# Optimization experiments

Hardware: AMD Instinct MI355X
Metric: run time of the kernel (lower is better)

## Reference

```python
import jax, jax.numpy as jnp
import numpy as np

# dims: T tokens, H hidden, E experts, I expert intermediate, K top-k
T, H, E, I, K = 2048, 1024, 64, 768, 8


def setup_inputs() -> dict:
    key = jax.random.key(0)
    k0, k1, k2, k3, k4 = jax.random.split(key, 5)
    s = 0.02  # init scale
    return {
        "hidden_states": jax.random.normal(k0, (T, H), jnp.float32),
        "w_router": jax.random.normal(k1, (E, H), jnp.float32) * s,   # gate (router) Linear, no bias
        "w_gate": jax.random.normal(k2, (E, I, H), jnp.float32) * s,  # per-expert gate_proj (out,in)
        "w_up": jax.random.normal(k3, (E, I, H), jnp.float32) * s,    # per-expert up_proj
        "w_down": jax.random.normal(k4, (E, H, I), jnp.float32) * s,  # per-expert down_proj
    }


def reference(hidden_states, w_router, w_gate, w_up, w_down):
    x = hidden_states  # (T, H)
    # --- router: softmax scores, top-k selection, renormalize (select_experts, softmax scoring) ---
    router_logits = jnp.einsum("th,eh->te", x, w_router)          # (T, E)
    probs = jax.nn.softmax(router_logits, axis=-1)
    topk_w, topk_ids = jax.lax.top_k(probs, K)                     # (T, K)
    topk_w = topk_w / jnp.sum(topk_w, axis=-1, keepdims=True)      # renormalize=True
    # scatter per-slot weights into a (T, E) combine matrix (zero for unselected experts)
    route = jnp.zeros((x.shape[0], E), x.dtype)
    route = route.at[jnp.arange(x.shape[0])[:, None], topk_ids].add(topk_w)
    # --- experts: SwiGLU MLP per expert, weighted combine (FusedMoE dispatch/combine) ---
    g = jnp.einsum("th,eih->tei", x, w_gate)                       # (T, E, I)
    u = jnp.einsum("th,eih->tei", x, w_up)
    h = jax.nn.silu(g) * u
    y = jnp.einsum("tei,ehi,te->th", h, w_down, route)             # weighted scatter-combine
    return y
```

## Files before the change

### kernel.cpp

```cpp
#include <hip/hip_runtime.h>
#include <hip/hip_bf16.h>
#include <cstdint>
#include <cstddef>

#define T_TOK 2048
#define H_DIM 1024
#define E_NUM 64
#define I_DIM 768
#define K_TOP 8

typedef __attribute__((ext_vector_type(8))) __bf16 bf16x8;
typedef __attribute__((ext_vector_type(8))) unsigned short u16x8;
typedef __attribute__((ext_vector_type(4))) float f32x4;
typedef unsigned short ushort_t;

__device__ __forceinline__ unsigned short f2bf(float f) {
  uint32_t u = __builtin_bit_cast(uint32_t, f);
  u += 0x7fffu + ((u >> 16) & 1u);
  return (unsigned short)(u >> 16);
}

__device__ __forceinline__ u16x8 cvt8b(f32x4 a, f32x4 b) {
  bf16x8 r;
  r[0] = (__bf16)a[0]; r[1] = (__bf16)a[1]; r[2] = (__bf16)a[2]; r[3] = (__bf16)a[3];
  r[4] = (__bf16)b[0]; r[5] = (__bf16)b[1]; r[6] = (__bf16)b[2]; r[7] = (__bf16)b[3];
  return __builtin_bit_cast(u16x8, r);
}

__device__ __forceinline__ void async16(const void* l, const void* g) {
  __builtin_amdgcn_global_load_lds(
      (const __attribute__((address_space(1))) unsigned int*)g,
      (__attribute__((address_space(3))) unsigned int*)l, 16, 0, 0);
}

__device__ __forceinline__ int xcd_decode(int wg0, int n_act) {
  int q = n_act >> 3, r = n_act & 7;
  int xcd = wg0 & 7, rank = wg0 >> 3;
  int cnt = q + (xcd < r ? 1 : 0);
  if (rank >= cnt) return -1;
  return (xcd < r ? xcd * (q + 1) : r * (q + 1) + (xcd - r) * q) + rank;
}

__global__ __launch_bounds__(256) void xcast_kernel(const float* __restrict__ x,
                                                    ushort_t* __restrict__ xb) {
  int i = blockIdx.x * 256 + threadIdx.x;
  const f32x4* s = (const f32x4*)(x + (size_t)i * 8);
  *(u16x8*)(xb + (size_t)i * 8) = cvt8b(s[0], s[1]);
}

__global__ __launch_bounds__(64) void router_kernel(
    const float* __restrict__ x, const float* __restrict__ wr,
    int* __restrict__ topk_id, float* __restrict__ topk_w,
    int* __restrict__ counts) {
  const int t0 = blockIdx.x * 4;
  const int e = threadIdx.x;
  const float4* wv = (const float4*)(wr + (size_t)e * H_DIM);
  const float4* xv0 = (const float4*)(x + (size_t)t0 * H_DIM);
  const float4* xv1 = (const float4*)(x + (size_t)(t0 + 1) * H_DIM);
  const float4* xv2 = (const float4*)(x + (size_t)(t0 + 2) * H_DIM);
  const float4* xv3 = (const float4*)(x + (size_t)(t0 + 3) * H_DIM);
  float acc0 = 0.f, acc1 = 0.f, acc2 = 0.f, acc3 = 0.f;
#pragma unroll 4
  for (int i = 0; i < H_DIM / 4; ++i) {
    float4 b = wv[i];
    float4 a0 = xv0[i], a1 = xv1[i], a2 = xv2[i], a3 = xv3[i];
    acc0 = fmaf(a0.x, b.x, fmaf(a0.y, b.y, fmaf(a0.z, b.z, fmaf(a0.w, b.w, acc0))));
    acc1 = fmaf(a1.x, b.x, fmaf(a1.y, b.y, fmaf(a1.z, b.z, fmaf(a1.w, b.w, acc1))));
    acc2 = fmaf(a2.x, b.x, fmaf(a2.y, b.y, fmaf(a2.z, b.z, fmaf(a2.w, b.w, acc2))));
    acc3 = fmaf(a3.x, b.x, fmaf(a3.y, b.y, fmaf(a3.z, b.z, fmaf(a3.w, b.w, acc3))));
  }
  float accs[4] = {acc0, acc1, acc2, acc3};
#pragma unroll 1
  for (int tt = 0; tt < 4; ++tt) {
    int t = t0 + tt;
    float acc = accs[tt];
    float m = acc;
    for (int o = 32; o; o >>= 1) m = fmaxf(m, __shfl_xor(m, o));
    float p = __expf(acc - m);
    float s = p;
    for (int o = 32; o; o >>= 1) s += __shfl_xor(s, o);
    p /= s;
    float v = p;
    int sid = 0;
    float sw = 0.f;
    for (int k = 0; k < K_TOP; ++k) {
      float bv = v;
      int bi = e;
      for (int o = 32; o; o >>= 1) {
        float ov = __shfl_xor(bv, o);
        int oi = __shfl_xor(bi, o);
        if (ov > bv || (ov == bv && oi < bi)) { bv = ov; bi = oi; }
      }
      if (e == k) { sid = bi; sw = bv; }
      if (e == bi) v = -1.f;
    }
    float ssum = (e < K_TOP) ? sw : 0.f;
    for (int o = 32; o; o >>= 1) ssum += __shfl_xor(ssum, o);
    if (e < K_TOP) {
      topk_id[t * K_TOP + e] = sid;
      topk_w[t * K_TOP + e] = sw / ssum;
      atomicAdd(&counts[sid], 1);
    }
  }
}

__global__ __launch_bounds__(64) void scan_kernel(
    const int* __restrict__ counts, int* __restrict__ offsets,
    int* __restrict__ cursor, int* __restrict__ tile_list,
    int* __restrict__ n_tiles) {
  int e = threadIdx.x;
  int ne = counts[e];
  int x = ne;
  for (int o = 1; o < 64; o <<= 1) {
    int v = __shfl_up(x, o);
    if (e >= o) x += v;
  }
  int excl = x - ne;
  offsets[e] = excl;
  cursor[e] = excl;
  int ntl = (ne + 127) >> 7;
  if (ntl > 3) ntl = 3;
  int y2 = ntl;
  for (int o = 1; o < 64; o <<= 1) {
    int v = __shfl_up(y2, o);
    if (e >= o) y2 += v;
  }
  int texcl = y2 - ntl;
  for (int m = 0; m < ntl; ++m) tile_list[texcl + m] = (e << 2) | m;
  if (e == 63) *n_tiles = texcl + ntl;
}

__global__ __launch_bounds__(256) void build_kernel(
    const int* __restrict__ topk_id, const float* __restrict__ topk_w,
    int* __restrict__ cursor, int* __restrict__ pair_token, float* __restrict__ pair_w) {
  int i = blockIdx.x * 256 + threadIdx.x;
  int t = i >> 3;
  int e = topk_id[i];
  int pos = atomicAdd(&cursor[e], 1);
  pair_token[pos] = t;
  pair_w[pos] = topk_w[i];
}


#define GU_NIT 32

__global__ __launch_bounds__(256, 3) void gemm_gu_kernel(
    const ushort_t* __restrict__ xb, const float* __restrict__ wg,
    const float* __restrict__ wu, const int* __restrict__ offsets,
    const int* __restrict__ counts, const int* __restrict__ pair_token,
    const int* __restrict__ tile_list, const int* __restrict__ n_tiles,
    ushort_t* __restrict__ h_buf) {
  int idx = xcd_decode(blockIdx.x, (*n_tiles) * 12);
  if (idx < 0) return;
  int tl = idx / 12, nt = idx - tl * 12;
  int ent = tile_list[tl];
  int e = ent >> 2, mt = ent & 3;
  int ne = counts[e], off = offsets[e];
  int ib = nt * 64;
  int vr = ne - mt * 128;
  if (vr <= 0) return;
  if (vr > 128) vr = 128;

  __shared__ __align__(16) ushort_t Xs[128 * 32];
  __shared__ __align__(16) ushort_t Gs[64 * 32];
  __shared__ __align__(16) ushort_t Us[64 * 32];
  __shared__ int sTok[128];

  const int tid = threadIdx.x;
  const int lane = tid & 63;
  const int wid = tid >> 6;
  if (tid < 128) {
    int p = mt * 128 + tid;
    sTok[tid] = pair_token[off + (p < ne ? p : ne - 1)];
  }
  __syncthreads();

  const ushort_t* xsrc[2];
  int xdst[2];
#pragma unroll
  for (int j = 0; j < 2; ++j) {
    int p = j * 256 + tid;
    int row = p >> 2, c = p & 3;
    xsrc[j] = xb + (size_t)sTok[row] * H_DIM + ((c ^ ((row >> 1) & 3)) << 3);
    xdst[j] = (j * 256 + wid * 64) * 8;
  }
  const int wrow = tid >> 2, wc = tid & 3;
  const float* gsrc = wg + ((size_t)e * I_DIM + ib + wrow) * H_DIM + wc * 8;
  const float* usrc = wu + ((size_t)e * I_DIM + ib + wrow) * H_DIM + wc * 8;
  const int wdst = (wrow * 4 + (wc ^ ((wrow >> 1) & 3))) * 8;

  const int wrM = wid >> 1, wrN = wid & 1;
  const int lrow = lane & 15, lk = lane >> 4;
  const bool wact = (wrM * 64) < vr;

  f32x4 accG[4][2], accU[4][2];
#pragma unroll
  for (int mi = 0; mi < 4; ++mi)
#pragma unroll
    for (int ni = 0; ni < 2; ++ni) {
      accG[mi][ni] = f32x4{0.f, 0.f, 0.f, 0.f};
      accU[mi][ni] = f32x4{0.f, 0.f, 0.f, 0.f};
    }

#pragma unroll 1
  for (int k = 0; k < GU_NIT; ++k) {
    const int k0 = k * 32;
    async16(&Xs[xdst[0]], xsrc[0] + k0);
    async16(&Xs[xdst[1]], xsrc[1] + k0);
    {
      f32x4 g0 = *(const f32x4*)(gsrc + k0);
      f32x4 g1 = *(const f32x4*)(gsrc + k0 + 4);
      f32x4 u0 = *(const f32x4*)(usrc + k0);
      f32x4 u1 = *(const f32x4*)(usrc + k0 + 4);
      *(u16x8*)&Gs[wdst] = cvt8b(g0, g1);
      *(u16x8*)&Us[wdst] = cvt8b(u0, u1);
    }
    __syncthreads();
    if (wact) {
      bf16x8 af[4];
#pragma unroll
      for (int mi = 0; mi < 4; ++mi) {
        int r = wrM * 64 + mi * 16 + lrow;
        af[mi] = __builtin_bit_cast(
            bf16x8, *(const u16x8*)&Xs[r * 32 + ((lk ^ ((r >> 1) & 3)) << 3)]);
      }
#pragma unroll
      for (int ni = 0; ni < 2; ++ni) {
        int br = wrN * 32 + ni * 16 + lrow;
        int ci = br * 32 + ((lk ^ ((br >> 1) & 3)) << 3);
        bf16x8 bg = __builtin_bit_cast(bf16x8, *(const u16x8*)&Gs[ci]);
        bf16x8 bu = __builtin_bit_cast(bf16x8, *(const u16x8*)&Us[ci]);
#pragma unroll
        for (int mi = 0; mi < 4; ++mi) {
          accG[mi][ni] = __builtin_amdgcn_mfma_f32_16x16x32_bf16(af[mi], bg, accG[mi][ni], 0, 0, 0);
          accU[mi][ni] = __builtin_amdgcn_mfma_f32_16x16x32_bf16(af[mi], bu, accU[mi][ni], 0, 0, 0);
        }
      }
    }
    __syncthreads();
  }

#pragma unroll
  for (int mi = 0; mi < 4; ++mi)
#pragma unroll
    for (int ni = 0; ni < 2; ++ni)
#pragma unroll
      for (int r = 0; r < 4; ++r) {
        int grow = wrM * 64 + mi * 16 + lk * 4 + r;
        if (grow < vr) {
          int col = ib + wrN * 32 + ni * 16 + lrow;
          float g = accG[mi][ni][r], u = accU[mi][ni][r];
          float hv = g / (1.f + __expf(-g)) * u;
          h_buf[(size_t)(off + mt * 128 + grow) * I_DIM + col] = f2bf(hv);
        }
      }
}

#define DN_NIT 24

__global__ __launch_bounds__(256, 3) void gemm_down_kernel(
    const ushort_t* __restrict__ h_buf, const float* __restrict__ wd,
    const int* __restrict__ offsets, const int* __restrict__ counts,
    const int* __restrict__ pair_token, const float* __restrict__ pair_w,
    const int* __restrict__ tile_list, const int* __restrict__ n_tiles,
    float* __restrict__ y) {
  int idx = xcd_decode(blockIdx.x, (*n_tiles) * 8);
  if (idx < 0) return;
  int tl = idx >> 3, nt = idx & 7;
  int ent = tile_list[tl];
  int e = ent >> 2, mt = ent & 3;
  int ne = counts[e], off = offsets[e];
  int hb = nt * 128;
  int vr = ne - mt * 128;
  if (vr <= 0) return;
  if (vr > 128) vr = 128;

  __shared__ __align__(16) ushort_t Ah[128 * 32];
  __shared__ __align__(16) ushort_t Bs[128 * 32];
  __shared__ int sTok[128];
  __shared__ float sPw[128];

  const int tid = threadIdx.x;
  const int lane = tid & 63;
  const int wid = tid >> 6;
  if (tid < 128) {
    int p = mt * 128 + tid;
    int ix = off + (p < ne ? p : ne - 1);
    sTok[tid] = pair_token[ix];
    sPw[tid] = pair_w[ix];
  }
  __syncthreads();

  const ushort_t* asrc[2];
  int adst[2];
#pragma unroll
  for (int j = 0; j < 2; ++j) {
    int p = j * 256 + tid;
    int row = p >> 2, c = p & 3;
    int pr = mt * 128 + row;
    int hr = off + (pr < ne ? pr : ne - 1);
    asrc[j] = h_buf + (size_t)hr * I_DIM + ((c ^ ((row >> 1) & 3)) << 3);
    adst[j] = (j * 256 + wid * 64) * 8;
  }
  const int brow = tid >> 1, bc0 = (tid & 1) * 2, bc1 = bc0 + 1;
  const float* bsrc = wd + ((size_t)e * H_DIM + hb + brow) * I_DIM + bc0 * 8;
  const int bdst0 = (brow * 4 + (bc0 ^ ((brow >> 1) & 3))) * 8;
  const int bdst1 = (brow * 4 + (bc1 ^ ((brow >> 1) & 3))) * 8;

  const int wrM = wid >> 1, wrN = wid & 1;
  const int lrow = lane & 15, lk = lane >> 4;
  const bool wact = (wrM * 64) < vr;

  f32x4 acc[4][4];
#pragma unroll
  for (int mi = 0; mi < 4; ++mi)
#pragma unroll
    for (int ni = 0; ni < 4; ++ni) acc[mi][ni] = f32x4{0.f, 0.f, 0.f, 0.f};

#pragma unroll 1
  for (int k = 0; k < DN_NIT; ++k) {
    const int k0 = k * 32;
    async16(&Ah[adst[0]], asrc[0] + k0);
    async16(&Ah[adst[1]], asrc[1] + k0);
    {
      f32x4 b0 = *(const f32x4*)(bsrc + k0);
      f32x4 b1 = *(const f32x4*)(bsrc + k0 + 4);
      f32x4 b2 = *(const f32x4*)(bsrc + k0 + 8);
      f32x4 b3 = *(const f32x4*)(bsrc + k0 + 12);
      *(u16x8*)&Bs[bdst0] = cvt8b(b0, b1);
      *(u16x8*)&Bs[bdst1] = cvt8b(b2, b3);
    }
    __syncthreads();
    if (wact) {
      bf16x8 af[4];
#pragma unroll
      for (int mi = 0; mi < 4; ++mi) {
        int r = wrM * 64 + mi * 16 + lrow;
        af[mi] = __builtin_bit_cast(
            bf16x8, *(const u16x8*)&Ah[r * 32 + ((lk ^ ((r >> 1) & 3)) << 3)]);
      }
#pragma unroll
      for (int ni = 0; ni < 4; ++ni) {
        int br = wrN * 64 + ni * 16 + lrow;
        bf16x8 bb = __builtin_bit_cast(
            bf16x8, *(const u16x8*)&Bs[br * 32 + ((lk ^ ((br >> 1) & 3)) << 3)]);
#pragma unroll
        for (int mi = 0; mi < 4; ++mi)
          acc[mi][ni] = __builtin_amdgcn_mfma_f32_16x16x32_bf16(af[mi], bb, acc[mi][ni], 0, 0, 0);
      }
    }
    __syncthreads();
  }

#pragma unroll
  for (int mi = 0; mi < 4; ++mi)
#pragma unroll
    for (int ni = 0; ni < 4; ++ni)
#pragma unroll
      for (int r = 0; r < 4; ++r) {
        int grow = wrM * 64 + mi * 16 + lk * 4 + r;
        if (grow < vr) {
          int col = hb + wrN * 64 + ni * 16 + lrow;
          float val = acc[mi][ni][r] * sPw[grow];
          unsafeAtomicAdd(&y[(size_t)sTok[grow] * H_DIM + col], val);
        }
      }
}

extern "C" void kernel_launch(void* const* d_in, const int* in_sizes, int n_in,
                              void* d_out, int out_size, void* d_ws, size_t ws_size,
                              hipStream_t stream) {
  const float* x  = (const float*)d_in[0];
  const float* wr = (const float*)d_in[1];
  const float* wg = (const float*)d_in[2];
  const float* wu = (const float*)d_in[3];
  const float* wd = (const float*)d_in[4];
  float* y = (float*)d_out;

  char* ws = (char*)d_ws;
  int* counts    = (int*)(ws + 0);
  int* offsets   = (int*)(ws + 256);
  int* cursor    = (int*)(ws + 512);
  int* n_tiles   = (int*)(ws + 768);
  int* tile_list = (int*)(ws + 1024);
  int*   topk_id    = (int*)(ws + 2048);
  float* topk_w     = (float*)(ws + 2048 + 1 * 65536);
  int*   pair_token = (int*)(ws + 2048 + 2 * 65536);
  float* pair_w     = (float*)(ws + 2048 + 3 * 65536);
  ushort_t* h_buf = (ushort_t*)(ws + 2048 + 4 * 65536);
  ushort_t* xb = (ushort_t*)(ws + 2048 + 4 * 65536 + (size_t)T_TOK * I_DIM * K_TOP * 2);

  hipMemsetAsync(counts, 0, 256, stream);
  hipMemsetAsync(y, 0, (size_t)T_TOK * H_DIM * sizeof(float), stream);

  xcast_kernel<<<(T_TOK * H_DIM / 8) / 256, 256, 0, stream>>>(x, xb);
  router_kernel<<<T_TOK / 4, 64, 0, stream>>>(x, wr, topk_id, topk_w, counts);
  scan_kernel<<<1, 64, 0, stream>>>(counts, offsets, cursor, tile_list, n_tiles);
  build_kernel<<<(T_TOK * K_TOP) / 256, 256, 0, stream>>>(topk_id, topk_w, cursor, pair_token, pair_w);
  gemm_gu_kernel<<<E_NUM * 3 * 12, 256, 0, stream>>>(
      xb, wg, wu, offsets, counts, pair_token, tile_list, n_tiles, h_buf);
  gemm_down_kernel<<<E_NUM * 3 * 8, 256, 0, stream>>>(
      h_buf, wd, offsets, counts, pair_token, pair_w, tile_list, n_tiles, y);
}
```

Before: 412.7 us.

## Enlarge MoE GEMM tiles to 256 rows with 512-thread blocks and double-buffered LDS

Both expert GEMM kernels now use 512-thread blocks covering 256 routed rows. Gate-up tiles are 128 intermediate columns (gate and up stacked into one B tile, combined through LDS in the epilogue), and down tiles are 256 hidden columns. The K loop is double-buffered: the next X/H async copy and the fp32 weight loads are issued before the MFMAs on the current buffer, leaving one barrier per iteration. The aim is fewer fp32 weight re-reads per expert, since fewer M-tiles cover each expert, plus overlap of loads with compute. In exchange, LDS use rises to about 66 KB and register pressure grows, which lowers occupancy, and tiles are more padded when experts have few tokens.

```diff
diff --git a/kernel.cpp b/kernel.cpp
--- a/kernel.cpp
+++ b/kernel.cpp
@@ -118,8 +118,8 @@
   int excl = x - ne;
   offsets[e] = excl;
   cursor[e] = excl;
-  int ntl = (ne + 127) >> 7;
-  if (ntl > 3) ntl = 3;
+  int ntl = (ne + 255) >> 8;
+  if (ntl > 2) ntl = 2;
   int y2 = ntl;
   for (int o = 1; o < 64; o <<= 1) {
     int v = __shfl_up(y2, o);
@@ -144,33 +144,36 @@
 
 #define GU_NIT 32
 
-__global__ __launch_bounds__(256, 3) void gemm_gu_kernel(
+__global__ __launch_bounds__(512) void gemm_gu_kernel(
     const ushort_t* __restrict__ xb, const float* __restrict__ wg,
     const float* __restrict__ wu, const int* __restrict__ offsets,
     const int* __restrict__ counts, const int* __restrict__ pair_token,
     const int* __restrict__ tile_list, const int* __restrict__ n_tiles,
     ushort_t* __restrict__ h_buf) {
-  int idx = xcd_decode(blockIdx.x, (*n_tiles) * 12);
+  int idx = xcd_decode(blockIdx.x, (*n_tiles) * 6);
   if (idx < 0) return;
-  int tl = idx / 12, nt = idx - tl * 12;
+  int tl = idx / 6, nt = idx - tl * 6;
   int ent = tile_list[tl];
   int e = ent >> 2, mt = ent & 3;
   int ne = counts[e], off = offsets[e];
-  int ib = nt * 64;
-  int vr = ne - mt * 128;
+  int ib = nt * 128;
+  int vr = ne - mt * 256;
   if (vr <= 0) return;
-  if (vr > 128) vr = 128;
-
-  __shared__ __align__(16) ushort_t Xs[128 * 32];
-  __shared__ __align__(16) ushort_t Gs[64 * 32];
-  __shared__ __align__(16) ushort_t Us[64 * 32];
-  __shared__ int sTok[128];
+  if (vr > 256) vr = 256;
+
+  __shared__ __align__(16) char L[66560];
+  ushort_t* Xs = (ushort_t*)L;
+  ushort_t* Bl = (ushort_t*)(L + 32768);
+  int* sTok = (int*)(L + 65536);
 
   const int tid = threadIdx.x;
   const int lane = tid & 63;
   const int wid = tid >> 6;
-  if (tid < 128) {
-    int p = mt * 128 + tid;
+  const int wrM = wid >> 2, wrN = wid & 3;
+  const int lrow = lane & 15, lk = lane >> 4;
+
+  if (tid < 256) {
+    int p = mt * 256 + tid;
     sTok[tid] = pair_token[off + (p < ne ? p : ne - 1)];
   }
   __syncthreads();
@@ -179,112 +182,152 @@
   int xdst[2];
 #pragma unroll
   for (int j = 0; j < 2; ++j) {
-    int p = j * 256 + tid;
+    int p = j * 512 + tid;
     int row = p >> 2, c = p & 3;
     xsrc[j] = xb + (size_t)sTok[row] * H_DIM + ((c ^ ((row >> 1) & 3)) << 3);
-    xdst[j] = (j * 256 + wid * 64) * 8;
-  }
-  const int wrow = tid >> 2, wc = tid & 3;
-  const float* gsrc = wg + ((size_t)e * I_DIM + ib + wrow) * H_DIM + wc * 8;
-  const float* usrc = wu + ((size_t)e * I_DIM + ib + wrow) * H_DIM + wc * 8;
-  const int wdst = (wrow * 4 + (wc ^ ((wrow >> 1) & 3))) * 8;
-
-  const int wrM = wid >> 1, wrN = wid & 1;
-  const int lrow = lane & 15, lk = lane >> 4;
-  const bool wact = (wrM * 64) < vr;
-
-  f32x4 accG[4][2], accU[4][2];
-#pragma unroll
-  for (int mi = 0; mi < 4; ++mi)
-#pragma unroll
-    for (int ni = 0; ni < 2; ++ni) {
-      accG[mi][ni] = f32x4{0.f, 0.f, 0.f, 0.f};
-      accU[mi][ni] = f32x4{0.f, 0.f, 0.f, 0.f};
-    }
+    xdst[j] = (j * 512 + wid * 64) * 8;
+  }
+  const int brow = tid >> 1;
+  const int cs0 = (tid & 1) * 2, cs1 = cs0 + 1;
+  const float* bq = (brow < 128)
+      ? wg + ((size_t)e * I_DIM + ib + brow) * H_DIM
+      : wu + ((size_t)e * I_DIM + ib + brow - 128) * H_DIM;
+  const float* bsrc0 = bq + cs0 * 8;
+  const float* bsrc1 = bq + cs1 * 8;
+  const int bd0 = (brow * 4 + (cs0 ^ ((brow >> 1) & 3))) * 8;
+  const int bd1 = (brow * 4 + (cs1 ^ ((brow >> 1) & 3))) * 8;
+
+  const bool wact = (wrM * 128) < vr;
+
+  f32x4 acc[8][4];
+#pragma unroll
+  for (int mi = 0; mi < 8; ++mi)
+#pragma unroll
+    for (int ni = 0; ni < 4; ++ni) acc[mi][ni] = f32x4{0.f, 0.f, 0.f, 0.f};
+
+#define GU_XDMA(B, K0)                                 \
+  do {                                                 \
+    async16(&Xs[(B) * 8192 + xdst[0]], xsrc[0] + (K0)); \
+    async16(&Xs[(B) * 8192 + xdst[1]], xsrc[1] + (K0)); \
+  } while (0)
+
+  f32x4 w0, w1, w2, w3;
+  GU_XDMA(0, 0);
+  w0 = *(const f32x4*)(bsrc0);
+  w1 = *(const f32x4*)(bsrc0 + 4);
+  w2 = *(const f32x4*)(bsrc1);
+  w3 = *(const f32x4*)(bsrc1 + 4);
+  *(u16x8*)&Bl[bd0] = cvt8b(w0, w1);
+  *(u16x8*)&Bl[bd1] = cvt8b(w2, w3);
+  asm volatile("s_waitcnt vmcnt(0) lgkmcnt(0)" ::: "memory");
+  __builtin_amdgcn_s_barrier();
 
 #pragma unroll 1
-  for (int k = 0; k < GU_NIT; ++k) {
-    const int k0 = k * 32;
-    async16(&Xs[xdst[0]], xsrc[0] + k0);
-    async16(&Xs[xdst[1]], xsrc[1] + k0);
-    {
-      f32x4 g0 = *(const f32x4*)(gsrc + k0);
-      f32x4 g1 = *(const f32x4*)(gsrc + k0 + 4);
-      f32x4 u0 = *(const f32x4*)(usrc + k0);
-      f32x4 u1 = *(const f32x4*)(usrc + k0 + 4);
-      *(u16x8*)&Gs[wdst] = cvt8b(g0, g1);
-      *(u16x8*)&Us[wdst] = cvt8b(u0, u1);
+  for (int K = 0; K < GU_NIT; ++K) {
+    const int B = K & 1;
+    if (K + 1 < GU_NIT) {
+      const int kn = (K + 1) * 32;
+      GU_XDMA(B ^ 1, kn);
+      w0 = *(const f32x4*)(bsrc0 + kn);
+      w1 = *(const f32x4*)(bsrc0 + kn + 4);
+      w2 = *(const f32x4*)(bsrc1 + kn);
+      w3 = *(const f32x4*)(bsrc1 + kn + 4);
+    }
+    if (wact) {
+      u16x8 bf[4];
+#pragma unroll
+      for (int ni = 0; ni < 4; ++ni) {
+        int br = wrN * 64 + ni * 16 + lrow;
+        bf[ni] = *(const u16x8*)&Bl[B * 8192 + br * 32 + ((lk ^ ((br >> 1) & 3)) << 3)];
+      }
+#pragma unroll
+      for (int mi = 0; mi < 8; ++mi) {
+        int r = wrM * 128 + mi * 16 + lrow;
+        u16x8 af = *(const u16x8*)&Xs[B * 8192 + r * 32 + ((lk ^ ((r >> 1) & 3)) << 3)];
+#pragma unroll
+        for (int ni = 0; ni < 4; ++ni)
+          acc[mi][ni] = __builtin_amdgcn_mfma_f32_16x16x32_bf16(
+              __builtin_bit_cast(bf16x8, af), __builtin_bit_cast(bf16x8, bf[ni]),
+              acc[mi][ni], 0, 0, 0);
+      }
+    }
+    asm volatile("s_waitcnt vmcnt(0)" ::: "memory");
+    if (K + 1 < GU_NIT) {
+      *(u16x8*)&Bl[(B ^ 1) * 8192 + bd0] = cvt8b(w0, w1);
+      *(u16x8*)&Bl[(B ^ 1) * 8192 + bd1] = cvt8b(w2, w3);
+    }
+    asm volatile("s_waitcnt lgkmcnt(0)" ::: "memory");
+    __builtin_amdgcn_s_barrier();
+  }
+#undef GU_XDMA
+
+  float* ex = (float*)L;
+#pragma unroll 1
+  for (int q = 0; q < 2; ++q) {
+    if (wrN == 2 + q) {
+#pragma unroll
+      for (int mi = 0; mi < 8; ++mi)
+#pragma unroll
+        for (int ni = 0; ni < 4; ++ni)
+#pragma unroll
+          for (int r = 0; r < 4; ++r)
+            ex[(wrM * 128 + mi * 16 + lk * 4 + r) * 64 + ni * 16 + lrow] = acc[mi][ni][r];
     }
     __syncthreads();
-    if (wact) {
-      bf16x8 af[4];
-#pragma unroll
-      for (int mi = 0; mi < 4; ++mi) {
-        int r = wrM * 64 + mi * 16 + lrow;
-        af[mi] = __builtin_bit_cast(
-            bf16x8, *(const u16x8*)&Xs[r * 32 + ((lk ^ ((r >> 1) & 3)) << 3)]);
-      }
-#pragma unroll
-      for (int ni = 0; ni < 2; ++ni) {
-        int br = wrN * 32 + ni * 16 + lrow;
-        int ci = br * 32 + ((lk ^ ((br >> 1) & 3)) << 3);
-        bf16x8 bg = __builtin_bit_cast(bf16x8, *(const u16x8*)&Gs[ci]);
-        bf16x8 bu = __builtin_bit_cast(bf16x8, *(const u16x8*)&Us[ci]);
-#pragma unroll
-        for (int mi = 0; mi < 4; ++mi) {
-          accG[mi][ni] = __builtin_amdgcn_mfma_f32_16x16x32_bf16(af[mi], bg, accG[mi][ni], 0, 0, 0);
-          accU[mi][ni] = __builtin_amdgcn_mfma_f32_16x16x32_bf16(af[mi], bu, accU[mi][ni], 0, 0, 0);
-        }
-      }
+    if (wrN == q) {
+#pragma unroll
+      for (int mi = 0; mi < 8; ++mi)
+#pragma unroll
+        for (int ni = 0; ni < 4; ++ni)
+#pragma unroll
+          for (int r = 0; r < 4; ++r) {
+            int grow = wrM * 128 + mi * 16 + lk * 4 + r;
+            if (grow < vr) {
+              float g = acc[mi][ni][r];
+              float u = ex[grow * 64 + ni * 16 + lrow];
+              float hv = g / (1.f + __expf(-g)) * u;
+              int col = ib + q * 64 + ni * 16 + lrow;
+              h_buf[(size_t)(off + mt * 256 + grow) * I_DIM + col] = f2bf(hv);
+            }
+          }
     }
     __syncthreads();
   }
-
-#pragma unroll
-  for (int mi = 0; mi < 4; ++mi)
-#pragma unroll
-    for (int ni = 0; ni < 2; ++ni)
-#pragma unroll
-      for (int r = 0; r < 4; ++r) {
-        int grow = wrM * 64 + mi * 16 + lk * 4 + r;
-        if (grow < vr) {
-          int col = ib + wrN * 32 + ni * 16 + lrow;
-          float g = accG[mi][ni][r], u = accU[mi][ni][r];
-          float hv = g / (1.f + __expf(-g)) * u;
-          h_buf[(size_t)(off + mt * 128 + grow) * I_DIM + col] = f2bf(hv);
-        }
-      }
 }
 
 #define DN_NIT 24
 
-__global__ __launch_bounds__(256, 3) void gemm_down_kernel(
+__global__ __launch_bounds__(512) void gemm_down_kernel(
     const ushort_t* __restrict__ h_buf, const float* __restrict__ wd,
     const int* __restrict__ offsets, const int* __restrict__ counts,
     const int* __restrict__ pair_token, const float* __restrict__ pair_w,
     const int* __restrict__ tile_list, const int* __restrict__ n_tiles,
     float* __restrict__ y) {
-  int idx = xcd_decode(blockIdx.x, (*n_tiles) * 8);
+  int idx = xcd_decode(blockIdx.x, (*n_tiles) * 4);
   if (idx < 0) return;
-  int tl = idx >> 3, nt = idx & 7;
+  int tl = idx >> 2, nt = idx & 3;
   int ent = tile_list[tl];
   int e = ent >> 2, mt = ent & 3;
   int ne = counts[e], off = offsets[e];
-  int hb = nt * 128;
-  int vr = ne - mt * 128;
+  int hb = nt * 256;
+  int vr = ne - mt * 256;
   if (vr <= 0) return;
-  if (vr > 128) vr = 128;
-
-  __shared__ __align__(16) ushort_t Ah[128 * 32];
-  __shared__ __align__(16) ushort_t Bs[128 * 32];
-  __shared__ int sTok[128];
-  __shared__ float sPw[128];
+  if (vr > 256) vr = 256;
+
+  __shared__ __align__(16) char L[67584];
+  ushort_t* Ah = (ushort_t*)L;
+  ushort_t* Bl = (ushort_t*)(L + 32768);
+  int* sTok = (int*)(L + 65536);
+  float* sPw = (float*)(L + 66560);
 
   const int tid = threadIdx.x;
   const int lane = tid & 63;
   const int wid = tid >> 6;
-  if (tid < 128) {
-    int p = mt * 128 + tid;
+  const int wrM = wid >> 2, wrN = wid & 3;
+  const int lrow = lane & 15, lk = lane >> 4;
+
+  if (tid < 256) {
+    int p = mt * 256 + tid;
     int ix = off + (p < ne ? p : ne - 1);
     sTok[tid] = pair_token[ix];
     sPw[tid] = pair_w[ix];
@@ -295,70 +338,92 @@
   int adst[2];
 #pragma unroll
   for (int j = 0; j < 2; ++j) {
-    int p = j * 256 + tid;
+    int p = j * 512 + tid;
     int row = p >> 2, c = p & 3;
-    int pr = mt * 128 + row;
+    int pr = mt * 256 + row;
     int hr = off + (pr < ne ? pr : ne - 1);
     asrc[j] = h_buf + (size_t)hr * I_DIM + ((c ^ ((row >> 1) & 3)) << 3);
-    adst[j] = (j * 256 + wid * 64) * 8;
-  }
-  const int brow = tid >> 1, bc0 = (tid & 1) * 2, bc1 = bc0 + 1;
-  const float* bsrc = wd + ((size_t)e * H_DIM + hb + brow) * I_DIM + bc0 * 8;
-  const int bdst0 = (brow * 4 + (bc0 ^ ((brow >> 1) & 3))) * 8;
-  const int bdst1 = (brow * 4 + (bc1 ^ ((brow >> 1) & 3))) * 8;
-
-  const int wrM = wid >> 1, wrN = wid & 1;
-  const int lrow = lane & 15, lk = lane >> 4;
-  const bool wact = (wrM * 64) < vr;
-
-  f32x4 acc[4][4];
-#pragma unroll
-  for (int mi = 0; mi < 4; ++mi)
+    adst[j] = (j * 512 + wid * 64) * 8;
+  }
+  const int brow = tid >> 1;
+  const int cs0 = (tid & 1) * 2, cs1 = cs0 + 1;
+  const float* bq = wd + ((size_t)e * H_DIM + hb + brow) * I_DIM;
+  const float* bsrc0 = bq + cs0 * 8;
+  const float* bsrc1 = bq + cs1 * 8;
+  const int bd0 = (brow * 4 + (cs0 ^ ((brow >> 1) & 3))) * 8;
+  const int bd1 = (brow * 4 + (cs1 ^ ((brow >> 1) & 3))) * 8;
+
+  const bool wact = (wrM * 128) < vr;
+
+  f32x4 acc[8][4];
+#pragma unroll
+  for (int mi = 0; mi < 8; ++mi)
 #pragma unroll
     for (int ni = 0; ni < 4; ++ni) acc[mi][ni] = f32x4{0.f, 0.f, 0.f, 0.f};
 
+#define DN_ADMA(B, K0)                                  \
+  do {                                                  \
+    async16(&Ah[(B) * 8192 + adst[0]], asrc[0] + (K0)); \
+    async16(&Ah[(B) * 8192 + adst[1]], asrc[1] + (K0)); \
+  } while (0)
+
+  f32x4 w0, w1, w2, w3;
+  DN_ADMA(0, 0);
+  w0 = *(const f32x4*)(bsrc0);
+  w1 = *(const f32x4*)(bsrc0 + 4);
+  w2 = *(const f32x4*)(bsrc1);
+  w3 = *(const f32x4*)(bsrc1 + 4);
+  *(u16x8*)&Bl[bd0] = cvt8b(w0, w1);
+  *(u16x8*)&Bl[bd1] = cvt8b(w2, w3);
+  asm volatile("s_waitcnt vmcnt(0) lgkmcnt(0)" ::: "memory");
+  __builtin_amdgcn_s_barrier();
+
 #pragma unroll 1
-  for (int k = 0; k < DN_NIT; ++k) {
-    const int k0 = k * 32;
-    async16(&Ah[adst[0]], asrc[0] + k0);
-    async16(&Ah[adst[1]], asrc[1] + k0);
-    {
-      f32x4 b0 = *(const f32x4*)(bsrc + k0);
-      f32x4 b1 = *(const f32x4*)(bsrc + k0 + 4);
-      f32x4 b2 = *(const f32x4*)(bsrc + k0 + 8);
-      f32x4 b3 = *(const f32x4*)(bsrc + k0 + 12);
-      *(u16x8*)&Bs[bdst0] = cvt8b(b0, b1);
-      *(u16x8*)&Bs[bdst1] = cvt8b(b2, b3);
-    }
-    __syncthreads();
+  for (int K = 0; K < DN_NIT; ++K) {
+    const int B = K & 1;
+    if (K + 1 < DN_NIT) {
+      const int kn = (K + 1) * 32;
+      DN_ADMA(B ^ 1, kn);
+      w0 = *(const f32x4*)(bsrc0 + kn);
+      w1 = *(const f32x4*)(bsrc0 + kn + 4);
+      w2 = *(const f32x4*)(bsrc1 + kn);
+      w3 = *(const f32x4*)(bsrc1 + kn + 4);
+    }
     if (wact) {
-      bf16x8 af[4];
-#pragma unroll
-      for (int mi = 0; mi < 4; ++mi) {
-        int r = wrM * 64 + mi * 16 + lrow;
-        af[mi] = __builtin_bit_cast(
-            bf16x8, *(const u16x8*)&Ah[r * 32 + ((lk ^ ((r >> 1) & 3)) << 3)]);
-      }
+      u16x8 bf[4];
 #pragma unroll
       for (int ni = 0; ni < 4; ++ni) {
         int br = wrN * 64 + ni * 16 + lrow;
-        bf16x8 bb = __builtin_bit_cast(
-            bf16x8, *(const u16x8*)&Bs[br * 32 + ((lk ^ ((br >> 1) & 3)) << 3)]);
-#pragma unroll
-        for (int mi = 0; mi < 4; ++mi)
-          acc[mi][ni] = __builtin_amdgcn_mfma_f32_16x16x32_bf16(af[mi], bb, acc[mi][ni], 0, 0, 0);
-      }
-    }
-    __syncthreads();
-  }
-
-#pragma unroll
-  for (int mi = 0; mi < 4; ++mi)
+        bf[ni] = *(const u16x8*)&Bl[B * 8192 + br * 32 + ((lk ^ ((br >> 1) & 3)) << 3)];
+      }
+#pragma unroll
+      for (int mi = 0; mi < 8; ++mi) {
+        int r = wrM * 128 + mi * 16 + lrow;
+        u16x8 af = *(const u16x8*)&Ah[B * 8192 + r * 32 + ((lk ^ ((r >> 1) & 3)) << 3)];
+#pragma unroll
+        for (int ni = 0; ni < 4; ++ni)
+          acc[mi][ni] = __builtin_amdgcn_mfma_f32_16x16x32_bf16(
+              __builtin_bit_cast(bf16x8, af), __builtin_bit_cast(bf16x8, bf[ni]),
+              acc[mi][ni], 0, 0, 0);
+      }
+    }
+    asm volatile("s_waitcnt vmcnt(0)" ::: "memory");
+    if (K + 1 < DN_NIT) {
+      *(u16x8*)&Bl[(B ^ 1) * 8192 + bd0] = cvt8b(w0, w1);
+      *(u16x8*)&Bl[(B ^ 1) * 8192 + bd1] = cvt8b(w2, w3);
+    }
+    asm volatile("s_waitcnt lgkmcnt(0)" ::: "memory");
+    __builtin_amdgcn_s_barrier();
+  }
+#undef DN_ADMA
+
+#pragma unroll
+  for (int mi = 0; mi < 8; ++mi)
 #pragma unroll
     for (int ni = 0; ni < 4; ++ni)
 #pragma unroll
       for (int r = 0; r < 4; ++r) {
-        int grow = wrM * 64 + mi * 16 + lk * 4 + r;
+        int grow = wrM * 128 + mi * 16 + lk * 4 + r;
         if (grow < vr) {
           int col = hb + wrN * 64 + ni * 16 + lrow;
           float val = acc[mi][ni][r] * sPw[grow];
@@ -397,8 +462,8 @@
   router_kernel<<<T_TOK / 4, 64, 0, stream>>>(x, wr, topk_id, topk_w, counts);
   scan_kernel<<<1, 64, 0, stream>>>(counts, offsets, cursor, tile_list, n_tiles);
   build_kernel<<<(T_TOK * K_TOP) / 256, 256, 0, stream>>>(topk_id, topk_w, cursor, pair_token, pair_w);
-  gemm_gu_kernel<<<E_NUM * 3 * 12, 256, 0, stream>>>(
+  gemm_gu_kernel<<<128 * 6, 512, 0, stream>>>(
       xb, wg, wu, offsets, counts, pair_token, tile_list, n_tiles, h_buf);
-  gemm_down_kernel<<<E_NUM * 3 * 8, 256, 0, stream>>>(
+  gemm_down_kernel<<<128 * 4, 512, 0, stream>>>(
       h_buf, wd, offsets, counts, pair_token, pair_w, tile_list, n_tiles, y);
 }
```

After: 584.8 us. +41.7%, slower.
